# Performance work log

Measured on AMD Instinct MI355X. Metric: run time of the kernel, lower is better.

The kernel has to match this reference:

```python
import jax, jax.numpy as jnp
import numpy as np

D_MODEL = 1024
NUM_HEADS = 16
HEAD_DIM = D_MODEL // NUM_HEADS


def setup_inputs() -> dict:
    key = jax.random.key(0)
    ks = jax.random.split(key, 9)
    s = 1.0 / np.sqrt(D_MODEL)
    x = jax.random.normal(ks[0], (4, 2048, D_MODEL), dtype=jnp.float32)
    Wq = jax.random.uniform(ks[1], (D_MODEL, D_MODEL), jnp.float32, -s, s)
    bq = jax.random.uniform(ks[2], (D_MODEL,), jnp.float32, -s, s)
    Wk = jax.random.uniform(ks[3], (D_MODEL, D_MODEL), jnp.float32, -s, s)
    bk = jax.random.uniform(ks[4], (D_MODEL,), jnp.float32, -s, s)
    Wv = jax.random.uniform(ks[5], (D_MODEL, D_MODEL), jnp.float32, -s, s)
    bv = jax.random.uniform(ks[6], (D_MODEL,), jnp.float32, -s, s)
    Wo = jax.random.uniform(ks[7], (D_MODEL, D_MODEL), jnp.float32, -s, s)
    bo = jax.random.uniform(ks[8], (D_MODEL,), jnp.float32, -s, s)
    return {"x": x, "Wq": Wq, "bq": bq, "Wk": Wk, "bk": bk,
            "Wv": Wv, "bv": bv, "Wo": Wo, "bo": bo}


def reference(x, Wq, bq, Wk, bk, Wv, bv, Wo, bo):
    B, S, D = x.shape
    H, hd = NUM_HEADS, HEAD_DIM
    # QKV projections (torch Linear: x @ W^T + b)
    q = (x @ Wq.T + bq).reshape(B, S, H, hd).transpose(0, 2, 1, 3)  # [B,H,S,hd]
    k = (x @ Wk.T + bk).reshape(B, S, H, hd).transpose(0, 2, 1, 3)
    v = (x @ Wv.T + bv).reshape(B, S, H, hd).transpose(0, 2, 1, 3)
    scores = jnp.einsum('bhqd,bhkd->bhqk', q, k) / jnp.sqrt(jnp.float32(hd))
    attn = jax.nn.softmax(scores, axis=-1)  # dropout is identity in eval
    ctx = jnp.einsum('bhqk,bhkd->bhqd', attn, v)
    ctx = ctx.transpose(0, 2, 1, 3).reshape(B, S, D)
    return ctx @ Wo.T + bo
```

## Files before the change

### kernel.cpp

```cpp
#include <hip/hip_runtime.h>

typedef __bf16 bf16;
typedef __bf16 bf16x4 __attribute__((ext_vector_type(4)));
typedef __bf16 bf16x8 __attribute__((ext_vector_type(8)));
typedef float  f32x4  __attribute__((ext_vector_type(4)));
typedef float  f32x16 __attribute__((ext_vector_type(16)));
typedef unsigned int u32x4v __attribute__((ext_vector_type(4)));

#define NB   4
#define SEQ  2048
#define DM   1024
#define NH   16
#define HD   64
#define BHN  (NB*NH)
#define MTOT (NB*SEQ)
#define ELEMS ((size_t)MTOT*DM)
#define WELEMS (DM*DM)
#define QSCALE 0.18033688011112042f

__device__ __forceinline__ void gload16(void* lds, const void* g) {
  __builtin_amdgcn_global_load_lds(
      (const __attribute__((address_space(1))) void*)g,
      (__attribute__((address_space(3))) void*)lds, 16, 0, 0);
}

__device__ __forceinline__ f32x4 mfma16(bf16x8 a, bf16x8 b, f32x4 c) {
  return __builtin_amdgcn_mfma_f32_16x16x32_bf16(a, b, c, 0, 0, 0);
}
__device__ __forceinline__ f32x16 mfma32(bf16x8 a, bf16x8 b, f32x16 c) {
  return __builtin_amdgcn_mfma_f32_32x32x16_bf16(a, b, c, 0, 0, 0);
}
__device__ __forceinline__ unsigned cvtpk(float lo, float hi) {
  unsigned r;
  asm("v_cvt_pk_bf16_f32 %0, %1, %2" : "=v"(r) : "v"(lo), "v"(hi));
  return r;
}
__device__ __forceinline__ float exp2a(float x) {
  float r;
  asm("v_exp_f32 %0, %1" : "=v"(r) : "v"(x));
  return r;
}

__global__ __launch_bounds__(256) void cvt_all(
    const float* __restrict__ x, bf16* __restrict__ xb,
    const float* __restrict__ w0, const float* __restrict__ w1,
    const float* __restrict__ w2, const float* __restrict__ w3,
    bf16* __restrict__ wb)
{
  int y = blockIdx.y;
  const float* src; bf16* dst; int nblk;
  if (y < 4) {
    src = (y == 0) ? w0 : (y == 1) ? w1 : (y == 2) ? w2 : w3;
    dst = wb + (size_t)y * WELEMS;
    nblk = WELEMS / 1024;
  } else {
    src = x; dst = xb; nblk = (int)(ELEMS / 1024);
  }
  if (blockIdx.x >= nblk) return;
  int i = blockIdx.x * 1024 + threadIdx.x * 4;
  f32x4 v = *(const f32x4*)(src + i);
  bf16x4 o;
#pragma unroll
  for (int j = 0; j < 4; j++) o[j] = (bf16)v[j];
  *(bf16x4*)(dst + i) = o;
}

#define GEMM_CORE(A_, W_)                                                      \
  __shared__ __align__(16) bf16 lds_a[128*32];                                 \
  __shared__ __align__(16) bf16 lds_b[128*32];                                 \
  const int K = 1024;                                                          \
  int tid = threadIdx.x, wid = tid >> 6, lane = tid & 63;                      \
  int m0 = blockIdx.y * 128, n0 = blockIdx.x * 128;                            \
  int wr = wid >> 1, wc = wid & 1;                                             \
  int c15 = lane & 15, hi = lane >> 4;                                         \
  int srow = lane >> 2, scol = (lane & 3) * 8;                                 \
  const bf16* gA = (A_) + (m0 + wid*32 + srow) * K + scol;                     \
  const bf16* gB = (W_) + (n0 + wid*32 + srow) * K + scol;                     \
  bf16* la = lds_a + wid*1024;                                                 \
  bf16* lb = lds_b + wid*1024;                                                 \
  f32x4 acc[4][4] = {};                                                        \
  for (int k0 = 0; k0 < K; k0 += 32) {                                         \
    __syncthreads();                                                           \
    gload16(la,       gA + k0);                                                \
    gload16(la + 512, gA + 16*K + k0);                                         \
    gload16(lb,       gB + k0);                                                \
    gload16(lb + 512, gB + 16*K + k0);                                         \
    __syncthreads();                                                           \
    bf16x8 af[4], bfr[4];                                                      \
    _Pragma("unroll")                                                          \
    for (int i = 0; i < 4; i++)                                                \
      af[i]  = *(const bf16x8*)(lds_a + (wr*64 + i*16 + c15)*32 + hi*8);       \
    _Pragma("unroll")                                                          \
    for (int i = 0; i < 4; i++)                                                \
      bfr[i] = *(const bf16x8*)(lds_b + (wc*64 + i*16 + c15)*32 + hi*8);       \
    _Pragma("unroll")                                                          \
    for (int mi = 0; mi < 4; mi++)                                             \
      _Pragma("unroll")                                                        \
      for (int ni = 0; ni < 4; ni++)                                           \
        acc[mi][ni] = mfma16(af[mi], bfr[ni], acc[mi][ni]);                    \
  }

__global__ __launch_bounds__(256) void gemm_qkv(
    const bf16* __restrict__ A, const bf16* __restrict__ Wb3,
    const float* __restrict__ bq, const float* __restrict__ bk,
    const float* __restrict__ bv,
    bf16* __restrict__ Qb, bf16* __restrict__ Kb, bf16* __restrict__ Vtb)
{
  int z = blockIdx.z;
  const bf16* W = Wb3 + (size_t)z * WELEMS;
  const float* bias = (z == 0) ? bq : (z == 1) ? bk : bv;
  GEMM_CORE(A, W)

  float sc = (z == 0) ? QSCALE : 1.0f;
#pragma unroll
  for (int mi = 0; mi < 4; mi++) {
#pragma unroll
    for (int ni = 0; ni < 4; ni++) {
      int col = n0 + wc*64 + ni*16 + c15;
      float bvv = bias[col];
      int row = m0 + wr*64 + mi*16 + hi*4;
      int b = row >> 11, s = row & 2047;
      int h = col >> 6,  d = col & 63;
      if (z < 2) {
        bf16* C = z ? Kb : Qb;
#pragma unroll
        for (int r = 0; r < 4; r++)
          C[((b*NH + h)*SEQ + (s + r))*HD + d] = (bf16)((acc[mi][ni][r] + bvv) * sc);
      } else {
        bf16x4 o;
#pragma unroll
        for (int r = 0; r < 4; r++) o[r] = (bf16)(acc[mi][ni][r] + bvv);
        *(bf16x4*)(Vtb + ((size_t)(b*NH + h)*HD + d)*SEQ + s) = o;
      }
    }
  }
}

__global__ __launch_bounds__(256) void gemm_out(
    const bf16* __restrict__ A, const bf16* __restrict__ W,
    const float* __restrict__ bias, float* __restrict__ C)
{
  GEMM_CORE(A, W)
#pragma unroll
  for (int mi = 0; mi < 4; mi++) {
#pragma unroll
    for (int ni = 0; ni < 4; ni++) {
      int col = n0 + wc*64 + ni*16 + c15;
      float bvv = bias[col];
      int row = m0 + wr*64 + mi*16 + hi*4;
#pragma unroll
      for (int r = 0; r < 4; r++)
        C[(row + r)*DM + col] = acc[mi][ni][r] + bvv;
    }
  }
}

__global__ __launch_bounds__(256, 2) void attn(
    const bf16* __restrict__ Q, const bf16* __restrict__ Kin,
    const bf16* __restrict__ Vt, bf16* __restrict__ ctx)
{
  __shared__ __align__(16) bf16 kt[2][128*64];
  __shared__ __align__(16) bf16 vt[2][64*128];

  int tid = threadIdx.x, wid = tid >> 6, lane = tid & 63;
  int l31 = lane & 31, hi = lane >> 5, l7 = lane & 7;

  int orig = blockIdx.y * gridDim.x + blockIdx.x;
  int swz  = (orig & 7) * 64 + (orig >> 3);
  int bh   = swz >> 3, q0 = (swz & 7) * 256;

  const bf16* Qp = Q   + (size_t)bh*SEQ*HD;
  const bf16* Kp = Kin + (size_t)bh*SEQ*HD;
  const bf16* Vp = Vt  + (size_t)bh*HD*SEQ;
  int qw = q0 + wid*64;

  bf16x8 qf[2][4];
#pragma unroll
  for (int qt = 0; qt < 2; qt++)
#pragma unroll
    for (int dblk = 0; dblk < 4; dblk++)
      qf[qt][dblk] = *(const bf16x8*)(Qp + (size_t)(qw + qt*32 + l31)*HD + dblk*16 + hi*8);

  f32x16 po[2][2]  = {};
  f32x16 posum[2]  = {};

  bf16x8 onesv;
#pragma unroll
  for (int j = 0; j < 8; j++) onesv[j] = (bf16)1.0f;

  int r8 = lane >> 3;
  int ck = (lane & 7) ^ r8;
  int r16 = lane >> 4, c16v = lane & 15;

#define STAGE(buf, kv0)                                                        \
  {                                                                            \
    _Pragma("unroll")                                                          \
    for (int op = 0; op < 4; op++) {                                           \
      int rk = wid*32 + op*8 + r8;                                             \
      gload16(&kt[buf][(wid*32 + op*8)*64],                                    \
              Kp + (size_t)((kv0) + rk)*HD + ck*8);                            \
      int rv = wid*16 + op*4 + r16;                                            \
      gload16(&vt[buf][(wid*16 + op*4)*128],                                   \
              Vp + (size_t)rv*SEQ + (kv0) + ((c16v ^ (rv & 7))*8));            \
    }                                                                          \
  }

  STAGE(0, 0);
  __syncthreads();

  for (int it = 0; it < SEQ/128; ++it) {
    int cur = it & 1;
    if (it < SEQ/128 - 1) STAGE(cur ^ 1, (it + 1) * 128);

#pragma unroll
    for (int sub = 0; sub < 2; sub++) {
      f32x16 st[2][2] = {};
      __builtin_amdgcn_s_setprio(1);
#pragma unroll
      for (int kvt = 0; kvt < 2; kvt++) {
        int rowb = (sub*64 + kvt*32 + l31) * 64;
#pragma unroll
        for (int dblk = 0; dblk < 4; dblk++) {
          bf16x8 kf = *(const bf16x8*)(&kt[cur][rowb + (((dblk*2 + hi) ^ l7) * 8)]);
          st[0][kvt] = mfma32(kf, qf[0][dblk], st[0][kvt]);
          st[1][kvt] = mfma32(kf, qf[1][dblk], st[1][kvt]);
        }
      }
      __builtin_amdgcn_s_setprio(0);

      bf16x8 pa[2][2][2];
#pragma unroll
      for (int qt = 0; qt < 2; qt++) {
#pragma unroll
        for (int kvt = 0; kvt < 2; kvt++)
#pragma unroll
          for (int i = 0; i < 16; i++)
            st[qt][kvt][i] = exp2a(st[qt][kvt][i]);
#pragma unroll
        for (int kvt = 0; kvt < 2; kvt++)
#pragma unroll
          for (int cp = 0; cp < 2; cp++) {
            int m0 = 2*cp, m1 = 2*cp + 1;
            unsigned w0a = cvtpk(st[qt][kvt][4*m0+0], st[qt][kvt][4*m0+1]);
            unsigned w1a = cvtpk(st[qt][kvt][4*m0+2], st[qt][kvt][4*m0+3]);
            unsigned w0b = cvtpk(st[qt][kvt][4*m1+0], st[qt][kvt][4*m1+1]);
            unsigned w1b = cvtpk(st[qt][kvt][4*m1+2], st[qt][kvt][4*m1+3]);
            asm("v_permlane32_swap_b32 %0, %1" : "+v"(w0a), "+v"(w0b));
            asm("v_permlane32_swap_b32 %0, %1" : "+v"(w1a), "+v"(w1b));
            pa[qt][kvt][cp] = __builtin_bit_cast(bf16x8, (u32x4v){w0a, w1a, w0b, w1b});
          }
      }

      __builtin_amdgcn_s_setprio(1);
#pragma unroll
      for (int dt = 0; dt < 2; dt++) {
        int rowb = (dt*32 + l31) * 128;
#pragma unroll
        for (int c = 0; c < 4; c++) {
          bf16x8 vf = *(const bf16x8*)(&vt[cur][rowb + ((sub*8 + ((c*2 + hi) ^ l7)) * 8)]);
          po[0][dt] = mfma32(pa[0][c >> 1][c & 1], vf, po[0][dt]);
          po[1][dt] = mfma32(pa[1][c >> 1][c & 1], vf, po[1][dt]);
        }
      }
#pragma unroll
      for (int c = 0; c < 4; c++) {
        posum[0] = mfma32(pa[0][c >> 1][c & 1], onesv, posum[0]);
        posum[1] = mfma32(pa[1][c >> 1][c & 1], onesv, posum[1]);
      }
      __builtin_amdgcn_s_setprio(0);
    }

    __syncthreads();
  }
#undef STAGE

  int b = bh >> 4, h = bh & 15;
#pragma unroll
  for (int qt = 0; qt < 2; qt++)
#pragma unroll
    for (int reg = 0; reg < 16; reg++) {
      int qq = (reg & 3) + 8*(reg >> 2) + 4*hi;
      float inv = 1.0f / posum[qt][reg];
      int s = qw + qt*32 + qq;
      bf16* dst = ctx + (size_t)(b*SEQ + s)*DM + h*HD + l31;
      dst[0]  = (bf16)(po[qt][0][reg] * inv);
      dst[32] = (bf16)(po[qt][1][reg] * inv);
    }
}

extern "C" void kernel_launch(void* const* d_in, const int* in_sizes, int n_in,
                              void* d_out, int out_size, void* d_ws, size_t ws_size,
                              hipStream_t stream)
{
  const float* x  = (const float*)d_in[0];
  const float* Wq = (const float*)d_in[1];
  const float* bq = (const float*)d_in[2];
  const float* Wk = (const float*)d_in[3];
  const float* bk = (const float*)d_in[4];
  const float* Wv = (const float*)d_in[5];
  const float* bv = (const float*)d_in[6];
  const float* Wo = (const float*)d_in[7];
  const float* bo = (const float*)d_in[8];

  bf16* ws  = (bf16*)d_ws;
  bf16* xb  = ws;
  bf16* Wb  = ws + ELEMS;
  bf16* Qb  = ws + ELEMS + 4*WELEMS;
  bf16* Kb  = Qb + ELEMS;
  bf16* Vtb = Kb + ELEMS;
  bf16* ctx = xb;

  dim3 blk(256);

  cvt_all<<<dim3(ELEMS/1024, 5), blk, 0, stream>>>(x, xb, Wq, Wk, Wv, Wo, Wb);
  gemm_qkv<<<dim3(DM/128, MTOT/128, 3), blk, 0, stream>>>(
      xb, Wb, bq, bk, bv, Qb, Kb, Vtb);
  attn<<<dim3(SEQ/256, BHN), blk, 0, stream>>>(Qb, Kb, Vtb, ctx);
  gemm_out<<<dim3(DM/128, MTOT/128), blk, 0, stream>>>(
      ctx, Wb + 3*WELEMS, bo, (float*)d_out);
}
```

Measured before the change: 189.5 us.

## Triple-buffer 64-wide KV tiles with vmcnt waits and one barrier per step

```diff
diff --git a/kernel.cpp b/kernel.cpp
--- a/kernel.cpp
+++ b/kernel.cpp
@@ -159,8 +159,8 @@
     const bf16* __restrict__ Q, const bf16* __restrict__ Kin,
     const bf16* __restrict__ Vt, bf16* __restrict__ ctx)
 {
-  __shared__ __align__(16) bf16 kt[2][128*64];
-  __shared__ __align__(16) bf16 vt[2][64*128];
+  __shared__ __align__(16) bf16 kt[3][64*64];
+  __shared__ __align__(16) bf16 vt[3][64*64];
 
   int tid = threadIdx.x, wid = tid >> 6, lane = tid & 63;
   int l31 = lane & 31, hi = lane >> 5, l7 = lane & 7;
@@ -181,96 +181,97 @@
     for (int dblk = 0; dblk < 4; dblk++)
       qf[qt][dblk] = *(const bf16x8*)(Qp + (size_t)(qw + qt*32 + l31)*HD + dblk*16 + hi*8);
 
-  f32x16 po[2][2]  = {};
-  f32x16 posum[2]  = {};
+  f32x16 po[2][2] = {};
+  f32x16 posum[2] = {};
 
   bf16x8 onesv;
 #pragma unroll
   for (int j = 0; j < 8; j++) onesv[j] = (bf16)1.0f;
 
   int r8 = lane >> 3;
-  int ck = (lane & 7) ^ r8;
-  int r16 = lane >> 4, c16v = lane & 15;
+  int c16s = (lane & 7) ^ r8;
 
 #define STAGE(buf, kv0)                                                        \
   {                                                                            \
     _Pragma("unroll")                                                          \
-    for (int op = 0; op < 4; op++) {                                           \
-      int rk = wid*32 + op*8 + r8;                                             \
-      gload16(&kt[buf][(wid*32 + op*8)*64],                                    \
-              Kp + (size_t)((kv0) + rk)*HD + ck*8);                            \
-      int rv = wid*16 + op*4 + r16;                                            \
-      gload16(&vt[buf][(wid*16 + op*4)*128],                                   \
-              Vp + (size_t)rv*SEQ + (kv0) + ((c16v ^ (rv & 7))*8));            \
+    for (int op = 0; op < 2; op++) {                                           \
+      int rowl = wid*16 + op*8 + r8;                                           \
+      gload16(&kt[buf][(wid*16 + op*8)*64], Kp + (size_t)((kv0) + rowl)*HD + c16s*8); \
+      gload16(&vt[buf][(wid*16 + op*8)*64], Vp + (size_t)rowl*SEQ + (kv0) + c16s*8);  \
     }                                                                          \
   }
 
+  const int NT = SEQ / 64;
   STAGE(0, 0);
-  __syncthreads();
-
-  for (int it = 0; it < SEQ/128; ++it) {
-    int cur = it & 1;
-    if (it < SEQ/128 - 1) STAGE(cur ^ 1, (it + 1) * 128);
-
-#pragma unroll
-    for (int sub = 0; sub < 2; sub++) {
-      f32x16 st[2][2] = {};
-      __builtin_amdgcn_s_setprio(1);
-#pragma unroll
-      for (int kvt = 0; kvt < 2; kvt++) {
-        int rowb = (sub*64 + kvt*32 + l31) * 64;
-#pragma unroll
-        for (int dblk = 0; dblk < 4; dblk++) {
-          bf16x8 kf = *(const bf16x8*)(&kt[cur][rowb + (((dblk*2 + hi) ^ l7) * 8)]);
-          st[0][kvt] = mfma32(kf, qf[0][dblk], st[0][kvt]);
-          st[1][kvt] = mfma32(kf, qf[1][dblk], st[1][kvt]);
+  STAGE(1, 64);
+
+  int cur = 0;
+  for (int it = 0; it < NT; ++it) {
+    if (it < NT - 1) { asm volatile("s_waitcnt vmcnt(4)" ::: "memory"); }
+    else             { asm volatile("s_waitcnt vmcnt(0)" ::: "memory"); }
+    __builtin_amdgcn_s_barrier();
+    asm volatile("" ::: "memory");
+    if (it + 2 < NT) {
+      int sb = (cur >= 1) ? cur - 1 : 2;
+      STAGE(sb, (it + 2) * 64);
+    }
+
+    f32x16 st[2][2] = {};
+    __builtin_amdgcn_s_setprio(1);
+#pragma unroll
+    for (int kvt = 0; kvt < 2; kvt++) {
+      int rowb = (kvt*32 + l31) * 64;
+#pragma unroll
+      for (int dblk = 0; dblk < 4; dblk++) {
+        bf16x8 kf = *(const bf16x8*)(&kt[cur][rowb + (((dblk*2 + hi) ^ l7) * 8)]);
+        st[0][kvt] = mfma32(kf, qf[0][dblk], st[0][kvt]);
+        st[1][kvt] = mfma32(kf, qf[1][dblk], st[1][kvt]);
+      }
+    }
+    __builtin_amdgcn_s_setprio(0);
+
+    bf16x8 pa[2][2][2];
+#pragma unroll
+    for (int qt = 0; qt < 2; qt++) {
+#pragma unroll
+      for (int kvt = 0; kvt < 2; kvt++)
+#pragma unroll
+        for (int i = 0; i < 16; i++)
+          st[qt][kvt][i] = exp2a(st[qt][kvt][i]);
+#pragma unroll
+      for (int kvt = 0; kvt < 2; kvt++)
+#pragma unroll
+        for (int cp = 0; cp < 2; cp++) {
+          int m0 = 2*cp, m1 = 2*cp + 1;
+          unsigned w0a = cvtpk(st[qt][kvt][4*m0+0], st[qt][kvt][4*m0+1]);
+          unsigned w1a = cvtpk(st[qt][kvt][4*m0+2], st[qt][kvt][4*m0+3]);
+          unsigned w0b = cvtpk(st[qt][kvt][4*m1+0], st[qt][kvt][4*m1+1]);
+          unsigned w1b = cvtpk(st[qt][kvt][4*m1+2], st[qt][kvt][4*m1+3]);
+          asm("v_permlane32_swap_b32 %0, %1" : "+v"(w0a), "+v"(w0b));
+          asm("v_permlane32_swap_b32 %0, %1" : "+v"(w1a), "+v"(w1b));
+          pa[qt][kvt][cp] = __builtin_bit_cast(bf16x8, (u32x4v){w0a, w1a, w0b, w1b});
         }
+    }
+
+    __builtin_amdgcn_s_setprio(1);
+#pragma unroll
+    for (int dt = 0; dt < 2; dt++) {
+      int rowb = (dt*32 + l31) * 64;
+#pragma unroll
+      for (int c = 0; c < 4; c++) {
+        bf16x8 vf = *(const bf16x8*)(&vt[cur][rowb + (((c*2 + hi) ^ l7) * 8)]);
+        po[0][dt] = mfma32(pa[0][c >> 1][c & 1], vf, po[0][dt]);
+        po[1][dt] = mfma32(pa[1][c >> 1][c & 1], vf, po[1][dt]);
       }
-      __builtin_amdgcn_s_setprio(0);
-
-      bf16x8 pa[2][2][2];
-#pragma unroll
-      for (int qt = 0; qt < 2; qt++) {
-#pragma unroll
-        for (int kvt = 0; kvt < 2; kvt++)
-#pragma unroll
-          for (int i = 0; i < 16; i++)
-            st[qt][kvt][i] = exp2a(st[qt][kvt][i]);
-#pragma unroll
-        for (int kvt = 0; kvt < 2; kvt++)
-#pragma unroll
-          for (int cp = 0; cp < 2; cp++) {
-            int m0 = 2*cp, m1 = 2*cp + 1;
-            unsigned w0a = cvtpk(st[qt][kvt][4*m0+0], st[qt][kvt][4*m0+1]);
-            unsigned w1a = cvtpk(st[qt][kvt][4*m0+2], st[qt][kvt][4*m0+3]);
-            unsigned w0b = cvtpk(st[qt][kvt][4*m1+0], st[qt][kvt][4*m1+1]);
-            unsigned w1b = cvtpk(st[qt][kvt][4*m1+2], st[qt][kvt][4*m1+3]);
-            asm("v_permlane32_swap_b32 %0, %1" : "+v"(w0a), "+v"(w0b));
-            asm("v_permlane32_swap_b32 %0, %1" : "+v"(w1a), "+v"(w1b));
-            pa[qt][kvt][cp] = __builtin_bit_cast(bf16x8, (u32x4v){w0a, w1a, w0b, w1b});
-          }
-      }
-
-      __builtin_amdgcn_s_setprio(1);
-#pragma unroll
-      for (int dt = 0; dt < 2; dt++) {
-        int rowb = (dt*32 + l31) * 128;
-#pragma unroll
-        for (int c = 0; c < 4; c++) {
-          bf16x8 vf = *(const bf16x8*)(&vt[cur][rowb + ((sub*8 + ((c*2 + hi) ^ l7)) * 8)]);
-          po[0][dt] = mfma32(pa[0][c >> 1][c & 1], vf, po[0][dt]);
-          po[1][dt] = mfma32(pa[1][c >> 1][c & 1], vf, po[1][dt]);
-        }
-      }
-#pragma unroll
-      for (int c = 0; c < 4; c++) {
-        posum[0] = mfma32(pa[0][c >> 1][c & 1], onesv, posum[0]);
-        posum[1] = mfma32(pa[1][c >> 1][c & 1], onesv, posum[1]);
-      }
-      __builtin_amdgcn_s_setprio(0);
-    }
-
-    __syncthreads();
+    }
+#pragma unroll
+    for (int c = 0; c < 4; c++) {
+      posum[0] = mfma32(pa[0][c >> 1][c & 1], onesv, posum[0]);
+      posum[1] = mfma32(pa[1][c >> 1][c & 1], onesv, posum[1]);
+    }
+    __builtin_amdgcn_s_setprio(0);
+
+    cur = (cur == 2) ? 0 : cur + 1;
   }
 #undef STAGE
 
```

After: 190.8 us. About the same (+0.7%).

## Replace QKV GEMM with 256x128-tile, 8-wave, double-buffered pipelined kernel

Applied to the files above, without the earlier changes.

```diff
diff --git a/kernel.cpp b/kernel.cpp
--- a/kernel.cpp
+++ b/kernel.cpp
@@ -100,29 +100,170 @@
         acc[mi][ni] = mfma16(af[mi], bfr[ni], acc[mi][ni]);                    \
   }
 
-__global__ __launch_bounds__(256) void gemm_qkv(
+__global__ __launch_bounds__(256) void gemm_out(
+    const bf16* __restrict__ A, const bf16* __restrict__ W,
+    const float* __restrict__ bias, float* __restrict__ C)
+{
+  GEMM_CORE(A, W)
+#pragma unroll
+  for (int mi = 0; mi < 4; mi++) {
+#pragma unroll
+    for (int ni = 0; ni < 4; ni++) {
+      int col = n0 + wc*64 + ni*16 + c15;
+      float bvv = bias[col];
+      int row = m0 + wr*64 + mi*16 + hi*4;
+#pragma unroll
+      for (int r = 0; r < 4; r++)
+        C[(row + r)*DM + col] = acc[mi][ni][r] + bvv;
+    }
+  }
+}
+
+__global__ __launch_bounds__(512, 2) void gemm_qkv256(
     const bf16* __restrict__ A, const bf16* __restrict__ Wb3,
     const float* __restrict__ bq, const float* __restrict__ bk,
     const float* __restrict__ bv,
     bf16* __restrict__ Qb, bf16* __restrict__ Kb, bf16* __restrict__ Vtb)
 {
-  int z = blockIdx.z;
-  const bf16* W = Wb3 + (size_t)z * WELEMS;
+  __shared__ __align__(16) bf16 la[2][256*64];
+  __shared__ __align__(16) bf16 lb[2][128*64];
+
+  const int K = 1024;
+  int tid = threadIdx.x, wid = tid >> 6, lane = tid & 63;
+  int wr = wid >> 1, wc = wid & 1;
+  int c15 = lane & 15, hi = lane >> 4, l7 = lane & 7;
+
+  int orig = blockIdx.x;
+  int swz  = (orig & 7) * 96 + (orig >> 3);
+  int by = swz & 31, bx = swz >> 5;
+  int m0 = by * 256, n0 = bx * 128;
+  int z  = n0 >> 10;
   const float* bias = (z == 0) ? bq : (z == 1) ? bk : bv;
-  GEMM_CORE(A, W)
-
-  float sc = (z == 0) ? QSCALE : 1.0f;
+
+  int r8 = lane >> 3;
+  int cu = (lane & 7) ^ r8;
+
+  const bf16* gA = A   + (size_t)m0 * K;
+  const bf16* gW = Wb3 + (size_t)n0 * K;
+
+#define STA(buf, h, kt)                                                        \
+  {                                                                            \
+    _Pragma("unroll")                                                          \
+    for (int op = 0; op < 2; op++) {                                           \
+      int rowl = (h)*128 + wid*16 + op*8 + r8;                                 \
+      gload16(&la[buf][((h)*128 + wid*16 + op*8)*64],                          \
+              gA + (size_t)rowl*K + (kt)*64 + cu*8);                           \
+    }                                                                          \
+  }
+#define STB(buf, kt)                                                           \
+  {                                                                            \
+    _Pragma("unroll")                                                          \
+    for (int op = 0; op < 2; op++) {                                           \
+      int rowl = wid*16 + op*8 + r8;                                           \
+      gload16(&lb[buf][(wid*16 + op*8)*64],                                    \
+              gW + (size_t)rowl*K + (kt)*64 + cu*8);                           \
+    }                                                                          \
+  }
+
+  f32x4 acc[4][4] = {};
+  const int NT = K / 64;
+
+  STB(0, 0);
+  STA(0, 0, 0);
+  STA(0, 1, 0);
+
+  for (int t = 0; t < NT; ++t) {
+    int cb = t & 1, nb = cb ^ 1;
+    asm volatile("s_waitcnt vmcnt(2)" ::: "memory");
+    __builtin_amdgcn_s_barrier();
+    asm volatile("" ::: "memory");
+
+    bf16x8 af0[2][2], af1[2][2], bf0[2][2], bf1[2][2];
+
+#pragma unroll
+    for (int mi = 0; mi < 2; mi++)
+#pragma unroll
+      for (int kk = 0; kk < 2; kk++)
+        af0[mi][kk] = *(const bf16x8*)(&la[cb][(wr*32 + mi*16 + c15)*64 + (((kk*4 + hi) ^ l7) * 8)]);
+#pragma unroll
+    for (int ni = 0; ni < 2; ni++)
+#pragma unroll
+      for (int kk = 0; kk < 2; kk++)
+        bf0[ni][kk] = *(const bf16x8*)(&lb[cb][(wc*64 + ni*16 + c15)*64 + (((kk*4 + hi) ^ l7) * 8)]);
+    if (t + 1 < NT) STB(nb, t + 1);
+    __builtin_amdgcn_s_setprio(1);
+#pragma unroll
+    for (int mi = 0; mi < 2; mi++)
+#pragma unroll
+      for (int ni = 0; ni < 2; ni++)
+#pragma unroll
+        for (int kk = 0; kk < 2; kk++)
+          acc[mi][ni] = mfma16(af0[mi][kk], bf0[ni][kk], acc[mi][ni]);
+    __builtin_amdgcn_s_setprio(0);
+
+#pragma unroll
+    for (int ni = 0; ni < 2; ni++)
+#pragma unroll
+      for (int kk = 0; kk < 2; kk++)
+        bf1[ni][kk] = *(const bf16x8*)(&lb[cb][(wc*64 + 32 + ni*16 + c15)*64 + (((kk*4 + hi) ^ l7) * 8)]);
+    if (t + 1 < NT) STA(nb, 0, t + 1);
+    __builtin_amdgcn_s_setprio(1);
+#pragma unroll
+    for (int mi = 0; mi < 2; mi++)
+#pragma unroll
+      for (int ni = 0; ni < 2; ni++)
+#pragma unroll
+        for (int kk = 0; kk < 2; kk++)
+          acc[mi][2 + ni] = mfma16(af0[mi][kk], bf1[ni][kk], acc[mi][2 + ni]);
+    __builtin_amdgcn_s_setprio(0);
+
+    if (t + 1 < NT) { asm volatile("s_waitcnt vmcnt(4)" ::: "memory"); }
+    else            { asm volatile("s_waitcnt vmcnt(0)" ::: "memory"); }
+    __builtin_amdgcn_s_barrier();
+    asm volatile("" ::: "memory");
+
+#pragma unroll
+    for (int mi = 0; mi < 2; mi++)
+#pragma unroll
+      for (int kk = 0; kk < 2; kk++)
+        af1[mi][kk] = *(const bf16x8*)(&la[cb][(128 + wr*32 + mi*16 + c15)*64 + (((kk*4 + hi) ^ l7) * 8)]);
+    if (t + 1 < NT) STA(nb, 1, t + 1);
+    __builtin_amdgcn_s_setprio(1);
+#pragma unroll
+    for (int mi = 0; mi < 2; mi++)
+#pragma unroll
+      for (int ni = 0; ni < 2; ni++)
+#pragma unroll
+        for (int kk = 0; kk < 2; kk++)
+          acc[2 + mi][2 + ni] = mfma16(af1[mi][kk], bf1[ni][kk], acc[2 + mi][2 + ni]);
+    __builtin_amdgcn_s_setprio(0);
+
+    __builtin_amdgcn_s_setprio(1);
+#pragma unroll
+    for (int mi = 0; mi < 2; mi++)
+#pragma unroll
+      for (int ni = 0; ni < 2; ni++)
+#pragma unroll
+        for (int kk = 0; kk < 2; kk++)
+          acc[2 + mi][ni] = mfma16(af1[mi][kk], bf0[ni][kk], acc[2 + mi][ni]);
+    __builtin_amdgcn_s_setprio(0);
+  }
+#undef STA
+#undef STB
+
 #pragma unroll
   for (int mi = 0; mi < 4; mi++) {
+    int rbase = m0 + ((mi < 2) ? (wr*32 + mi*16) : (128 + wr*32 + (mi - 2)*16)) + hi*4;
 #pragma unroll
     for (int ni = 0; ni < 4; ni++) {
-      int col = n0 + wc*64 + ni*16 + c15;
-      float bvv = bias[col];
-      int row = m0 + wr*64 + mi*16 + hi*4;
-      int b = row >> 11, s = row & 2047;
-      int h = col >> 6,  d = col & 63;
+      int n  = n0 + wc*64 + ni*16 + c15;
+      int cz = n & 1023;
+      float bvv = bias[cz];
+      int h = cz >> 6, d = cz & 63;
+      int b = rbase >> 11, s = rbase & 2047;
       if (z < 2) {
         bf16* C = z ? Kb : Qb;
+        float sc = z ? 1.0f : QSCALE;
 #pragma unroll
         for (int r = 0; r < 4; r++)
           C[((b*NH + h)*SEQ + (s + r))*HD + d] = (bf16)((acc[mi][ni][r] + bvv) * sc);
@@ -132,25 +273,6 @@
         for (int r = 0; r < 4; r++) o[r] = (bf16)(acc[mi][ni][r] + bvv);
         *(bf16x4*)(Vtb + ((size_t)(b*NH + h)*HD + d)*SEQ + s) = o;
       }
-    }
-  }
-}
-
-__global__ __launch_bounds__(256) void gemm_out(
-    const bf16* __restrict__ A, const bf16* __restrict__ W,
-    const float* __restrict__ bias, float* __restrict__ C)
-{
-  GEMM_CORE(A, W)
-#pragma unroll
-  for (int mi = 0; mi < 4; mi++) {
-#pragma unroll
-    for (int ni = 0; ni < 4; ni++) {
-      int col = n0 + wc*64 + ni*16 + c15;
-      float bvv = bias[col];
-      int row = m0 + wr*64 + mi*16 + hi*4;
-#pragma unroll
-      for (int r = 0; r < 4; r++)
-        C[(row + r)*DM + col] = acc[mi][ni][r] + bvv;
     }
   }
 }
@@ -310,12 +432,10 @@
   bf16* Vtb = Kb + ELEMS;
   bf16* ctx = xb;
 
-  dim3 blk(256);
-
-  cvt_all<<<dim3(ELEMS/1024, 5), blk, 0, stream>>>(x, xb, Wq, Wk, Wv, Wo, Wb);
-  gemm_qkv<<<dim3(DM/128, MTOT/128, 3), blk, 0, stream>>>(
+  cvt_all<<<dim3(ELEMS/1024, 5), dim3(256), 0, stream>>>(x, xb, Wq, Wk, Wv, Wo, Wb);
+  gemm_qkv256<<<dim3(768), dim3(512), 0, stream>>>(
       xb, Wb, bq, bk, bv, Qb, Kb, Vtb);
-  attn<<<dim3(SEQ/256, BHN), blk, 0, stream>>>(Qb, Kb, Vtb, ctx);
-  gemm_out<<<dim3(DM/128, MTOT/128), blk, 0, stream>>>(
+  attn<<<dim3(SEQ/256, BHN), dim3(256), 0, stream>>>(Qb, Kb, Vtb, ctx);
+  gemm_out<<<dim3(DM/128, MTOT/128), dim3(256), 0, stream>>>(
       ctx, Wb + 3*WELEMS, bo, (float*)d_out);
 }
```

Measured after the change: 196.4 us. +3.7%, slower.
